# Performance work log

Hardware: AMD Instinct MI355X
Metric: run time of the kernel (lower is better)

## Reference

```python
import jax, jax.numpy as jnp
import numpy as np

THRESH = 0.5
MARGIN = 0.1
SCALE_POS = 2.0
SCALE_NEG = 40.0
EPS = 1e-5


def setup_inputs() -> dict:
    key = jax.random.key(0)
    k1, k2 = jax.random.split(key)
    B, D, NUM_CLASSES = 4096, 512, 512
    feats = jax.random.normal(k1, (B, D), dtype=jnp.float32)
    feats = feats / jnp.linalg.norm(feats, axis=1, keepdims=True)  # unit-norm embeddings
    labels = jax.random.randint(k2, (B,), 0, NUM_CLASSES, dtype=jnp.int64)
    return {"feats": feats, "labels": labels, "label_num": 26}


def reference(feats, labels, label_num):
    B = feats.shape[0]
    sim = feats @ feats.T  # [B, B]
    same = labels[:, None] == labels[None, :]
    pos_m = same & (sim < 1.0 - EPS)      # pos_pair_ mask per row
    neg_m = ~same                         # neg_pair_ mask per row
    has_pos = pos_m.any(axis=1)
    has_neg = neg_m.any(axis=1)
    min_pos = jnp.min(jnp.where(pos_m, sim, jnp.inf), axis=1)
    max_neg = jnp.max(jnp.where(neg_m, sim, -jnp.inf), axis=1)
    pos_thr = jnp.where(has_pos, min_pos, jnp.float32(0.2))  # fallback when no pos pairs
    neg_thr = jnp.where(has_neg, max_neg, jnp.float32(0.8))  # fallback when no neg pairs
    # mined pairs (same semantics as the per-row boolean filtering)
    neg_pair = neg_m & (sim + MARGIN > pos_thr[:, None])
    pos_pair = pos_m & (sim - MARGIN < neg_thr[:, None])
    valid = pos_pair.any(axis=1) & neg_pair.any(axis=1) & (jnp.arange(B) < B - label_num)
    # masked log-sum-exp style reductions (exp of -inf on masked entries -> 0)
    pos_sum = jnp.sum(jnp.exp(jnp.where(pos_pair, -SCALE_POS * (sim - THRESH), -jnp.inf)), axis=1)
    neg_sum = jnp.sum(jnp.exp(jnp.where(neg_pair, SCALE_NEG * (sim - THRESH), -jnp.inf)), axis=1)
    per_row = (1.0 / SCALE_POS) * jnp.log1p(pos_sum) + (1.0 / SCALE_NEG) * jnp.log1p(neg_sum)
    return jnp.sum(jnp.where(valid, per_row, 0.0)) / B
```

## Files before the change

kernel.cpp:

```cpp
#include <hip/hip_runtime.h>
#include <stdint.h>

#define BN 4096
#define DK 512
#define THRESH 0.5f
#define MARGIN 0.1f

typedef __attribute__((ext_vector_type(4))) float f32x4;
typedef __attribute__((ext_vector_type(8))) unsigned short ushort8;
typedef __attribute__((ext_vector_type(2))) unsigned long long ulong2_t;

__device__ __forceinline__ unsigned short f2bf(float f) {
    unsigned u = __float_as_uint(f);
    u += 0x7FFFu + ((u >> 16) & 1u);
    return (unsigned short)(u >> 16);
}
__device__ __forceinline__ float bf2f(unsigned short b) {
    return __uint_as_float((unsigned)b << 16);
}

__device__ __forceinline__ unsigned char f2fp8(float x) {
    float a = fabsf(x);
    unsigned s = (__float_as_uint(x) >> 24) & 0x80u;
    if (a >= 448.f) return (unsigned char)(s | 0x7E);
    if (a < 0.015625f) {
        int m = (int)(a * 512.0f + 0.5f);
        return (unsigned char)(s | m);
    }
    unsigned u = __float_as_uint(a);
    u += 0x0FFFFFu + ((u >> 20) & 1u);
    unsigned e = (u >> 23) - 127u + 7u;
    unsigned m = (u >> 20) & 7u;
    if (e >= 16u) return (unsigned char)(s | 0x7E);
    return (unsigned char)(s | (e << 3) | m);
}

__device__ __forceinline__ void async_cp16(void* lds, const void* g) {
    __builtin_amdgcn_global_load_lds(
        (const __attribute__((address_space(1))) void*)g,
        (__attribute__((address_space(3))) void*)lds,
        16, 0, 0);
}

__global__ void cvt_kernel(const float4* __restrict__ in, uchar4* __restrict__ out,
                           float* __restrict__ loss_out) {
    int i = blockIdx.x * blockDim.x + threadIdx.x;
    float4 v = in[i];
    uchar4 o;
    o.x = f2fp8(v.x); o.y = f2fp8(v.y); o.z = f2fp8(v.z); o.w = f2fp8(v.w);
    out[i] = o;
    if (blockIdx.x == 0 && threadIdx.x == 0) loss_out[0] = 0.f;
}

__global__ __launch_bounds__(256, 4) void ms_gemm(
    const unsigned char* __restrict__ Fb,
    unsigned short* __restrict__ simb)
{
    __shared__ __align__(16) unsigned char SMEMB[32768];
    unsigned char* As = SMEMB;
    unsigned char* Bs = SMEMB + 16384;
    unsigned short* SMEM = (unsigned short*)SMEMB;

    const int t    = threadIdx.x;
    const int lane = t & 63;
    const int w    = t >> 6;
    const int wr   = w >> 1, wc = w & 1;
    const int quad = lane >> 4;
    const int cIdx = lane & 15;

    int l = blockIdx.x, by = 0;
    while (l >= 32 - by) { l -= (32 - by); ++by; }
    const int bx = by + l;
    const int rowBase = by * 128;
    const int colBase = bx * 128;
    const bool diag = (by == bx);
    const unsigned char* Bsel = diag ? As : Bs;

    f32x4 acc[4][4];
#pragma unroll
    for (int i = 0; i < 4; ++i)
#pragma unroll
        for (int j = 0; j < 4; ++j) acc[i][j] = (f32x4){0.f, 0.f, 0.f, 0.f};

    for (int k0 = 0; k0 < DK; k0 += 128) {
#pragma unroll
        for (int it = 0; it < 4; ++it) {
            const int id = it * 256 + t;
            const int r  = id >> 3;
            const int gc = (id & 7) ^ (r & 7);
            async_cp16(As + id * 16,
                       Fb + (size_t)(rowBase + r) * DK + k0 + gc * 16);
        }
        if (!diag) {
#pragma unroll
            for (int it = 0; it < 4; ++it) {
                const int id = it * 256 + t;
                const int r  = id >> 3;
                const int gc = (id & 7) ^ (r & 7);
                async_cp16(Bs + id * 16,
                           Fb + (size_t)(colBase + r) * DK + k0 + gc * 16);
            }
        }
        __syncthreads();

#pragma unroll
        for (int kk = 0; kk < 4; ++kk) {
            long af[4], bg[4];
#pragma unroll
            for (int im = 0; im < 4; ++im) {
                int r = wr * 64 + im * 16 + cIdx;
                int u = kk * 4 + quad;
                int p = (u >> 1) ^ (r & 7);
                af[im] = *reinterpret_cast<const long*>(
                    &As[r * 128 + p * 16 + (u & 1) * 8]);
            }
#pragma unroll
            for (int jn = 0; jn < 4; ++jn) {
                int c = wc * 64 + jn * 16 + cIdx;
                int u = kk * 4 + quad;
                int p = (u >> 1) ^ (c & 7);
                bg[jn] = *reinterpret_cast<const long*>(
                    &Bsel[c * 128 + p * 16 + (u & 1) * 8]);
            }
#pragma unroll
            for (int im = 0; im < 4; ++im)
#pragma unroll
                for (int jn = 0; jn < 4; ++jn)
                    acc[im][jn] = __builtin_amdgcn_mfma_f32_16x16x32_fp8_fp8(
                        af[im], bg[jn], acc[im][jn], 0, 0, 0);
        }
        __syncthreads();
    }

#pragma unroll
    for (int im = 0; im < 4; ++im)
#pragma unroll
        for (int rg = 0; rg < 4; ++rg) {
            const int grow = rowBase + wr * 64 + im * 16 + quad * 4 + rg;
            unsigned short* dst = simb + (size_t)grow * BN + colBase + wc * 64 + cIdx;
#pragma unroll
            for (int jn = 0; jn < 4; ++jn)
                dst[jn * 16] = f2bf(acc[im][jn][rg]);
        }

    if (diag) return;

#pragma unroll
    for (int im = 0; im < 4; ++im)
#pragma unroll
        for (int jn = 0; jn < 4; ++jn) {
            ushort4 v;
            v.x = f2bf(acc[im][jn][0]);
            v.y = f2bf(acc[im][jn][1]);
            v.z = f2bf(acc[im][jn][2]);
            v.w = f2bf(acc[im][jn][3]);
            const int c  = wc * 64 + jn * 16 + cIdx;
            const int r  = wr * 64 + im * 16 + quad * 4;
            const int r8 = r >> 3;
            const int ri = r & 7;
            *reinterpret_cast<ushort4*>(
                &SMEM[c * 128 + ((r8 ^ (c & 15)) << 3) + ri]) = v;
        }
    __syncthreads();

    const int lch = t & 7;
    const int trw = t >> 3;
#pragma unroll
    for (int it = 0; it < 4; ++it) {
        const int tr = it * 32 + trw;
        const int q1 = lch ^ (tr & 15);
        const int q2 = (lch + 8) ^ (tr & 15);
        ushort8 a = *reinterpret_cast<const ushort8*>(&SMEM[tr * 128 + q1 * 8]);
        ushort8 b = *reinterpret_cast<const ushort8*>(&SMEM[tr * 128 + q2 * 8]);
        unsigned short* dst = simb + (size_t)(colBase + tr) * BN + rowBase;
        *reinterpret_cast<ushort8*>(&dst[lch * 8])       = a;
        *reinterpret_cast<ushort8*>(&dst[(lch + 8) * 8]) = b;
    }
}

__global__ __launch_bounds__(256) void ms_rows(
    const unsigned short* __restrict__ simb,
    const int* __restrict__ labels,
    const int* __restrict__ label_num,
    float* __restrict__ out)
{
    __shared__ int   labT[8][512];
    __shared__ float bsum[4];

    const int t    = threadIdx.x;
    const int lane = t & 63;
    const int w    = t >> 6;

    for (int i = t; i < BN; i += 256) labT[i & 7][i >> 3] = labels[i];
    __syncthreads();

    const int lim = BN - label_num[0];
    const int row = blockIdx.x * 4 + w;
    const int lr  = labT[row & 7][row >> 3];
    const ulong2_t* rq = (const ulong2_t*)(simb + (size_t)row * BN);

    ulong2_t q[8];
    uint64_t mpos = 0, mneg = 0;
    float mn = INFINITY, mx = -INFINITY;
#pragma unroll
    for (int j = 0; j < 8; ++j) {
        q[j] = rq[j * 64 + lane];
        const int c8 = j * 64 + lane;
#pragma unroll
        for (int e = 0; e < 8; ++e) {
            const int col = c8 * 8 + e;
            const float s = bf2f((unsigned short)(q[j][e >> 2] >> ((e & 3) * 16)));
            const bool same = (labT[e][c8] == lr);
            const bool pos  = same && (col != row);
            if (pos)   mn = fminf(mn, s);
            if (!same) mx = fmaxf(mx, s);
            mpos |= (uint64_t)pos << (j * 8 + e);
            mneg |= (uint64_t)(!same && (s > 0.125f)) << (j * 8 + e);
        }
    }
#pragma unroll
    for (int off = 1; off < 64; off <<= 1) {
        mn = fminf(mn, __shfl_xor(mn, off, 64));
        mx = fmaxf(mx, __shfl_xor(mx, off, 64));
    }
    const bool hasP = (mn < 1e30f);
    const bool hasN = (mx > -1e30f);
    const float tP = hasP ? mn : 0.2f;
    const float tN = hasN ? mx : 0.8f;

    float ps = 0.f, ns = 0.f;
#pragma unroll
    for (int j = 0; j < 8; ++j) {
        unsigned bm = (unsigned)((mpos >> (j * 8)) & 0xFFull)
                    | ((unsigned)((mneg >> (j * 8)) & 0xFFull) << 8);
        while (bm) {
            const int k = __builtin_ctz(bm);
            bm &= bm - 1;
            const uint64_t h = (k & 4) ? q[j][1] : q[j][0];
            const float s = bf2f((unsigned short)(h >> ((k & 3) * 16)));
            const bool isneg = k >= 8;
            const bool ok  = isneg ? (s + MARGIN > tP) : (s - MARGIN < tN);
            const float a  = isneg ? 40.0f * (s - THRESH) : -2.0f * (s - THRESH);
            const float v  = ok ? __expf(a) : 0.f;
            if (isneg) ns += v; else ps += v;
        }
    }
#pragma unroll
    for (int off = 1; off < 64; off <<= 1) {
        ps += __shfl_xor(ps, off, 64);
        ns += __shfl_xor(ns, off, 64);
    }
    const bool vP = hasP && (mn - MARGIN < tN);
    const bool vN = hasN && (mx + MARGIN > tP);
    float wsum = 0.f;
    if (lane == 0 && vP && vN && row < lim)
        wsum = 0.5f * log1pf(ps) + 0.025f * log1pf(ns);

    if (lane == 0) bsum[w] = wsum;
    __syncthreads();
    if (t == 0)
        atomicAdd(out, (bsum[0] + bsum[1] + bsum[2] + bsum[3]) * (1.0f / (float)BN));
}

extern "C" void kernel_launch(void* const* d_in, const int* in_sizes, int n_in,
                              void* d_out, int out_size, void* d_ws, size_t ws_size,
                              hipStream_t stream)
{
    const float* feats     = (const float*)d_in[0];
    const int*   labels    = (const int*)d_in[1];
    const int*   label_num = (const int*)d_in[2];
    float*       out       = (float*)d_out;

    char* ws = (char*)d_ws;
    unsigned char*  Fb   = (unsigned char*)ws;
    unsigned short* simb = (unsigned short*)(ws + 4u * 1024u * 1024u);

    cvt_kernel<<<2048, 256, 0, stream>>>((const float4*)feats, (uchar4*)Fb, out);

    ms_gemm<<<528, 256, 0, stream>>>(Fb, simb);

    ms_rows<<<1024, 256, 0, stream>>>(simb, labels, label_num, out);
}
```

Before: 105.4 us.

## Use 32x32x64 scaled fp8 MFMA with direct global operand loads

Replaces the 16x16x32 fp8 MFMA tile loop with the gfx950 scaled 32x32x64 f8f6f4 MFMA, using neutral scales. Operands are now loaded straight from global memory into registers, dropping the LDS staging, swizzled async copies and per-k-step barriers. LDS is kept only for the transposed write of the mirrored tile. This halves the MFMA instruction count and removes sync overhead. The cost is loss of LDS data reuse: each wave re-reads its A/B rows from global or L2, and there is no explicit prefetch or overlap.

```diff
diff --git a/kernel.cpp b/kernel.cpp
--- a/kernel.cpp
+++ b/kernel.cpp
@@ -6,7 +6,9 @@
 #define THRESH 0.5f
 #define MARGIN 0.1f
 
-typedef __attribute__((ext_vector_type(4))) float f32x4;
+typedef __attribute__((ext_vector_type(4)))  int   i32x4;
+typedef __attribute__((ext_vector_type(8)))  int   i32x8;
+typedef __attribute__((ext_vector_type(16))) float f32x16;
 typedef __attribute__((ext_vector_type(8))) unsigned short ushort8;
 typedef __attribute__((ext_vector_type(2))) unsigned long long ulong2_t;
 
@@ -33,13 +35,6 @@
     unsigned m = (u >> 20) & 7u;
     if (e >= 16u) return (unsigned char)(s | 0x7E);
     return (unsigned char)(s | (e << 3) | m);
-}
-
-__device__ __forceinline__ void async_cp16(void* lds, const void* g) {
-    __builtin_amdgcn_global_load_lds(
-        (const __attribute__((address_space(1))) void*)g,
-        (__attribute__((address_space(3))) void*)lds,
-        16, 0, 0);
 }
 
 __global__ void cvt_kernel(const float4* __restrict__ in, uchar4* __restrict__ out,
@@ -56,17 +51,14 @@
     const unsigned char* __restrict__ Fb,
     unsigned short* __restrict__ simb)
 {
-    __shared__ __align__(16) unsigned char SMEMB[32768];
-    unsigned char* As = SMEMB;
-    unsigned char* Bs = SMEMB + 16384;
-    unsigned short* SMEM = (unsigned short*)SMEMB;
+    __shared__ __align__(16) unsigned short SMEM[128 * 128];
 
     const int t    = threadIdx.x;
     const int lane = t & 63;
     const int w    = t >> 6;
     const int wr   = w >> 1, wc = w & 1;
-    const int quad = lane >> 4;
-    const int cIdx = lane & 15;
+    const int l31  = lane & 31;
+    const int kh   = lane >> 5;
 
     int l = blockIdx.x, by = 0;
     while (l >= 32 - by) { l -= (32 - by); ++by; }
@@ -74,93 +66,84 @@
     const int rowBase = by * 128;
     const int colBase = bx * 128;
     const bool diag = (by == bx);
-    const unsigned char* Bsel = diag ? As : Bs;
-
-    f32x4 acc[4][4];
-#pragma unroll
-    for (int i = 0; i < 4; ++i)
-#pragma unroll
-        for (int j = 0; j < 4; ++j) acc[i][j] = (f32x4){0.f, 0.f, 0.f, 0.f};
-
-    for (int k0 = 0; k0 < DK; k0 += 128) {
-#pragma unroll
-        for (int it = 0; it < 4; ++it) {
-            const int id = it * 256 + t;
-            const int r  = id >> 3;
-            const int gc = (id & 7) ^ (r & 7);
-            async_cp16(As + id * 16,
-                       Fb + (size_t)(rowBase + r) * DK + k0 + gc * 16);
-        }
-        if (!diag) {
-#pragma unroll
-            for (int it = 0; it < 4; ++it) {
-                const int id = it * 256 + t;
-                const int r  = id >> 3;
-                const int gc = (id & 7) ^ (r & 7);
-                async_cp16(Bs + id * 16,
-                           Fb + (size_t)(colBase + r) * DK + k0 + gc * 16);
+
+    const unsigned char* aP[2];
+    const unsigned char* bP[2];
+#pragma unroll
+    for (int im = 0; im < 2; ++im)
+        aP[im] = Fb + (size_t)(rowBase + wr * 64 + im * 32 + l31) * DK + kh * 32;
+#pragma unroll
+    for (int jn = 0; jn < 2; ++jn)
+        bP[jn] = Fb + (size_t)(colBase + wc * 64 + jn * 32 + l31) * DK + kh * 32;
+
+    f32x16 acc[2][2];
+#pragma unroll
+    for (int i = 0; i < 2; ++i)
+#pragma unroll
+        for (int j = 0; j < 2; ++j)
+#pragma unroll
+            for (int e = 0; e < 16; ++e) acc[i][j][e] = 0.f;
+
+#pragma unroll
+    for (int ks = 0; ks < 8; ++ks) {
+        i32x8 af[2], bg[2];
+#pragma unroll
+        for (int im = 0; im < 2; ++im) {
+            i32x4 lo = *reinterpret_cast<const i32x4*>(aP[im] + ks * 64);
+            i32x4 hi = *reinterpret_cast<const i32x4*>(aP[im] + ks * 64 + 16);
+            af[im] = __builtin_shufflevector(lo, hi, 0, 1, 2, 3, 4, 5, 6, 7);
+        }
+#pragma unroll
+        for (int jn = 0; jn < 2; ++jn) {
+            i32x4 lo = *reinterpret_cast<const i32x4*>(bP[jn] + ks * 64);
+            i32x4 hi = *reinterpret_cast<const i32x4*>(bP[jn] + ks * 64 + 16);
+            bg[jn] = __builtin_shufflevector(lo, hi, 0, 1, 2, 3, 4, 5, 6, 7);
+        }
+#pragma unroll
+        for (int im = 0; im < 2; ++im)
+#pragma unroll
+            for (int jn = 0; jn < 2; ++jn)
+                acc[im][jn] = __builtin_amdgcn_mfma_scale_f32_32x32x64_f8f6f4(
+                    af[im], bg[jn], acc[im][jn],
+                    0, 0,
+                    0, 0x7F7F7F7F,
+                    0, 0x7F7F7F7F);
+    }
+
+#pragma unroll
+    for (int im = 0; im < 2; ++im)
+#pragma unroll
+        for (int g = 0; g < 4; ++g)
+#pragma unroll
+            for (int rg = 0; rg < 4; ++rg) {
+                const int grow = rowBase + wr * 64 + im * 32 + g * 8 + kh * 4 + rg;
+                unsigned short* dst = simb + (size_t)grow * BN + colBase + wc * 64 + l31;
+#pragma unroll
+                for (int jn = 0; jn < 2; ++jn)
+                    dst[jn * 32] = f2bf(acc[im][jn][g * 4 + rg]);
             }
-        }
-        __syncthreads();
-
-#pragma unroll
-        for (int kk = 0; kk < 4; ++kk) {
-            long af[4], bg[4];
-#pragma unroll
-            for (int im = 0; im < 4; ++im) {
-                int r = wr * 64 + im * 16 + cIdx;
-                int u = kk * 4 + quad;
-                int p = (u >> 1) ^ (r & 7);
-                af[im] = *reinterpret_cast<const long*>(
-                    &As[r * 128 + p * 16 + (u & 1) * 8]);
+
+    if (diag) return;
+
+    __syncthreads();
+#pragma unroll
+    for (int im = 0; im < 2; ++im)
+#pragma unroll
+        for (int jn = 0; jn < 2; ++jn)
+#pragma unroll
+            for (int g = 0; g < 4; ++g) {
+                ushort4 v;
+                v.x = f2bf(acc[im][jn][g * 4 + 0]);
+                v.y = f2bf(acc[im][jn][g * 4 + 1]);
+                v.z = f2bf(acc[im][jn][g * 4 + 2]);
+                v.w = f2bf(acc[im][jn][g * 4 + 3]);
+                const int c  = wc * 64 + jn * 32 + l31;
+                const int r  = wr * 64 + im * 32 + g * 8 + kh * 4;
+                const int r8 = r >> 3;
+                const int ri = r & 7;
+                *reinterpret_cast<ushort4*>(
+                    &SMEM[c * 128 + ((r8 ^ (c & 15)) << 3) + ri]) = v;
             }
-#pragma unroll
-            for (int jn = 0; jn < 4; ++jn) {
-                int c = wc * 64 + jn * 16 + cIdx;
-                int u = kk * 4 + quad;
-                int p = (u >> 1) ^ (c & 7);
-                bg[jn] = *reinterpret_cast<const long*>(
-                    &Bsel[c * 128 + p * 16 + (u & 1) * 8]);
-            }
-#pragma unroll
-            for (int im = 0; im < 4; ++im)
-#pragma unroll
-                for (int jn = 0; jn < 4; ++jn)
-                    acc[im][jn] = __builtin_amdgcn_mfma_f32_16x16x32_fp8_fp8(
-                        af[im], bg[jn], acc[im][jn], 0, 0, 0);
-        }
-        __syncthreads();
-    }
-
-#pragma unroll
-    for (int im = 0; im < 4; ++im)
-#pragma unroll
-        for (int rg = 0; rg < 4; ++rg) {
-            const int grow = rowBase + wr * 64 + im * 16 + quad * 4 + rg;
-            unsigned short* dst = simb + (size_t)grow * BN + colBase + wc * 64 + cIdx;
-#pragma unroll
-            for (int jn = 0; jn < 4; ++jn)
-                dst[jn * 16] = f2bf(acc[im][jn][rg]);
-        }
-
-    if (diag) return;
-
-#pragma unroll
-    for (int im = 0; im < 4; ++im)
-#pragma unroll
-        for (int jn = 0; jn < 4; ++jn) {
-            ushort4 v;
-            v.x = f2bf(acc[im][jn][0]);
-            v.y = f2bf(acc[im][jn][1]);
-            v.z = f2bf(acc[im][jn][2]);
-            v.w = f2bf(acc[im][jn][3]);
-            const int c  = wc * 64 + jn * 16 + cIdx;
-            const int r  = wr * 64 + im * 16 + quad * 4;
-            const int r8 = r >> 3;
-            const int ri = r & 7;
-            *reinterpret_cast<ushort4*>(
-                &SMEM[c * 128 + ((r8 ^ (c & 15)) << 3) + ri]) = v;
-        }
     __syncthreads();
 
     const int lch = t & 7;
```

Measured after the change: 116.9 us. 10.9% more time.
